# Kernel tuning notes

Hardware: AMD Instinct MI355X
Metric: run time of the kernel (lower is better)

Reference implementation:

```python
import jax, jax.numpy as jnp
import numpy as np

D_MODEL, NUM_HEADS, ROPE_DIM = 256, 8, 16
B_GRAPHS, N_MAX = 16, 512


def _make_batch():
    # ragged graph sizes between 256 and 512 atoms; contiguous, sorted ids
    sizes = np.array([256 + (i * 256) // 15 for i in range(B_GRAPHS)], dtype=np.int64)
    return np.repeat(np.arange(B_GRAPHS), sizes)  # total N = 6137


def setup_inputs() -> dict:
    key = jax.random.key(0)
    ks = jax.random.split(key, 6)
    batch_np = _make_batch()
    N = int(batch_np.shape[0])
    x = jax.random.normal(ks[0], (N, D_MODEL), jnp.float32)
    pos = jax.random.normal(ks[1], (N, 3), jnp.float32) * 3.0
    W_qkv = jax.random.normal(ks[2], (D_MODEL, 3 * D_MODEL), jnp.float32) / np.sqrt(D_MODEL).astype(np.float32)
    W_out = jax.random.normal(ks[3], (D_MODEL, D_MODEL), jnp.float32) / np.sqrt(D_MODEL).astype(np.float32)
    rope_freqs = jax.random.normal(ks[4], (ROPE_DIM,), jnp.float32) * 0.1
    W_rope = jax.random.normal(ks[5], (ROPE_DIM, NUM_HEADS), jnp.float32) / np.sqrt(ROPE_DIM).astype(np.float32)
    gamma = jnp.ones((D_MODEL,), jnp.float32)
    beta = jnp.zeros((D_MODEL,), jnp.float32)
    return {"x": x, "pos": pos, "batch": jnp.asarray(batch_np, jnp.int32),
            "W_qkv": W_qkv, "W_out": W_out, "rope_freqs": rope_freqs,
            "W_rope": W_rope, "gamma": gamma, "beta": beta,
            "B": B_GRAPHS, "n_max": N_MAX}


def _forward(x, pos, W_qkv, W_out, rope_freqs, W_rope, gamma, beta, batch, B, n_max):
    N, d = x.shape
    H = W_rope.shape[1]
    hd = d // H
    scale = hd ** -0.5
    # pad ragged graphs to [B, n_max] via vectorized scatter (batch is sorted)
    sizes = jax.ops.segment_sum(jnp.ones((N,), jnp.int32), batch, num_segments=B)
    offsets = jnp.concatenate([jnp.zeros((1,), jnp.int32), jnp.cumsum(sizes)[:-1].astype(jnp.int32)])
    pidx = jnp.arange(N, dtype=jnp.int32) - offsets[batch]  # position within graph
    x_pad = jnp.zeros((B, n_max, d), x.dtype).at[batch, pidx].set(x)
    pos_pad = jnp.zeros((B, n_max, 3), pos.dtype).at[batch, pidx].set(pos)
    pad = jnp.ones((B, n_max), bool).at[batch, pidx].set(False)  # True = padding
    # multi-head self-attention on scalar channel
    qkv = x_pad @ W_qkv  # [B, n, 3d]
    q, k, v = jnp.split(qkv, 3, axis=-1)
    heads = lambda t: t.reshape(B, n_max, H, hd).transpose(0, 2, 1, 3)  # [B,H,n,hd]
    q, k, v = heads(q), heads(k), heads(v)
    logits = jnp.einsum('bhid,bhjd->bhij', q, k) * scale
    # Euclidean RoPE distance bias: rope_proj(cos(|omega| * ||r_i - r_j||))
    diff = pos_pad[:, :, None, :] - pos_pad[:, None, :, :]  # [B,n,n,3]
    sq = jnp.sum(diff * diff, axis=-1)
    dist = jnp.where(sq > 0, jnp.sqrt(jnp.where(sq > 0, sq, 1.0)), 0.0)  # safe norm
    fourier = jnp.cos(dist[..., None] * jnp.abs(rope_freqs))  # [B,n,n,r]
    bias = jnp.einsum('bijr,rh->bhij', fourier, W_rope)
    pair_pad = (pad[:, :, None] | pad[:, None, :])[:, None]  # [B,1,n,n]
    bias = jnp.where(pair_pad, 0.0, bias)
    logits = jnp.where(pad[:, None, None, :], -1e9, logits + bias)
    attn = jax.nn.softmax(logits, axis=-1)
    out = jnp.einsum('bhij,bhjd->bhid', attn, v)
    out = out.transpose(0, 2, 1, 3).reshape(B, n_max, d) @ W_out
    out_flat = out[batch, pidx]  # gather back to flat node list
    # residual + LayerNorm (eps = 1e-5)
    y = x + out_flat
    mu = jnp.mean(y, axis=-1, keepdims=True)
    var = jnp.mean((y - mu) ** 2, axis=-1, keepdims=True)
    return gamma * (y - mu) * jax.lax.rsqrt(var + 1e-5) + beta


def reference(x, pos, batch, W_qkv, W_out, rope_freqs, W_rope, gamma, beta, B, n_max):
    return _forward(x, pos, W_qkv, W_out, rope_freqs, W_rope, gamma, beta, batch, B, n_max)
```

## Files before the change

### kernel.cpp

```cpp
#include <hip/hip_runtime.h>
#include <hip/hip_bf16.h>

typedef __hip_bfloat16 bf16;
typedef short bf16x8 __attribute__((ext_vector_type(8)));
typedef float f32x4 __attribute__((ext_vector_type(4)));

#define NGRAPH 16
#define QSCALE 0.17677669529663687f
#define VT_LD 8192

__device__ __forceinline__ bf16x8 ldcvt8(const float* p) {
  float4 u = *(const float4*)p, v = *(const float4*)(p + 4);
  __align__(16) bf16 tmp[8];
  tmp[0] = __float2bfloat16(u.x); tmp[1] = __float2bfloat16(u.y);
  tmp[2] = __float2bfloat16(u.z); tmp[3] = __float2bfloat16(u.w);
  tmp[4] = __float2bfloat16(v.x); tmp[5] = __float2bfloat16(v.y);
  tmp[6] = __float2bfloat16(v.z); tmp[7] = __float2bfloat16(v.w);
  return *(const bf16x8*)tmp;
}

__global__ __launch_bounds__(256) void k_pre(const float* __restrict__ Wqkv,
                                             const float* __restrict__ Wout,
                                             const int* __restrict__ batch,
                                             bf16* __restrict__ Wqkv_t,
                                             bf16* __restrict__ Wout_t,
                                             int* __restrict__ offs, int N) {
  __shared__ float ld[64][65];
  int bid = blockIdx.x, t = threadIdx.x;
  int c = t & 63, r0 = t >> 6;
  if (bid < 48) {
    int k0 = (bid & 3) * 64, n0 = (bid >> 2) * 64;
    #pragma unroll
    for (int r = r0; r < 64; r += 4) ld[r][c] = Wqkv[(size_t)(k0 + r) * 768 + n0 + c];
    __syncthreads();
    #pragma unroll
    for (int r = r0; r < 64; r += 4)
      Wqkv_t[(size_t)(n0 + r) * 256 + k0 + c] = __float2bfloat16(ld[c][r]);
  } else if (bid < 64) {
    int b2 = bid - 48;
    int k0 = (b2 & 3) * 64, n0 = (b2 >> 2) * 64;
    #pragma unroll
    for (int r = r0; r < 64; r += 4) ld[r][c] = Wout[(size_t)(k0 + r) * 256 + n0 + c];
    __syncthreads();
    #pragma unroll
    for (int r = r0; r < 64; r += 4)
      Wout_t[(size_t)(n0 + r) * 256 + k0 + c] = __float2bfloat16(ld[c][r]);
  } else {
    for (int i = t; i < N; i += 256) {
      if (i == 0) { offs[0] = 0; offs[NGRAPH] = N; }
      else if (batch[i] != batch[i - 1]) offs[batch[i]] = i;
    }
  }
}

__global__ __launch_bounds__(256) void k_gemm(const float* __restrict__ x,
                                              const bf16* __restrict__ Wqkv_t,
                                              const int* __restrict__ batch,
                                              const int* __restrict__ offs,
                                              bf16* __restrict__ QKVb,
                                              bf16* __restrict__ VT,
                                              int N, int MBm) {
  __shared__ float tr[64][65];
  __shared__ int rowcol[64];
  int t = threadIdx.x, bid = blockIdx.x;
  int w = t >> 6, l = t & 63, fr = l & 15, fq = l >> 4;
  int m0 = (bid % MBm) * 64, n0 = (bid / MBm) * 64;
  bool isV = (n0 >= 512);
  if (isV && t < 64) {
    int m = m0 + t; if (m > N - 1) m = N - 1;
    int b = batch[m];
    rowcol[t] = b * 512 + (m - offs[b]);
  }
  int arow = m0 + w * 16 + fr; if (arow > N - 1) arow = N - 1;
  bf16x8 af[8];
  #pragma unroll
  for (int kt = 0; kt < 8; ++kt)
    af[kt] = ldcvt8(x + (size_t)arow * 256 + kt * 32 + fq * 8);
  f32x4 acc[4];
  #pragma unroll
  for (int nt = 0; nt < 4; ++nt) acc[nt] = (f32x4){0.f, 0.f, 0.f, 0.f};
  #pragma unroll
  for (int nt = 0; nt < 4; ++nt) {
    int brow = n0 + nt * 16 + fr;
    #pragma unroll
    for (int kt = 0; kt < 8; ++kt) {
      bf16x8 bf_ = *(const bf16x8*)(Wqkv_t + (size_t)brow * 256 + kt * 32 + fq * 8);
      acc[nt] = __builtin_amdgcn_mfma_f32_16x16x32_bf16(af[kt], bf_, acc[nt], 0, 0, 0);
    }
  }
  #pragma unroll
  for (int nt = 0; nt < 4; ++nt) {
    int col = n0 + nt * 16 + fr;
    float sc = (col < 256) ? QSCALE : 1.f;
    #pragma unroll
    for (int rr = 0; rr < 4; ++rr) {
      int m = m0 + w * 16 + fq * 4 + rr;
      if (m < N) QKVb[(size_t)m * 768 + col] = __float2bfloat16(acc[nt][rr] * sc);
    }
  }
  if (isV) {
    #pragma unroll
    for (int nt = 0; nt < 4; ++nt)
      #pragma unroll
      for (int rr = 0; rr < 4; ++rr)
        tr[nt * 16 + fr][w * 16 + fq * 4 + rr] = acc[nt][rr];
    __syncthreads();
    int c = t >> 2, r0 = (t & 3) * 16;
    int dg = (n0 - 512) + c;
    #pragma unroll
    for (int i = 0; i < 16; ++i) {
      int r = r0 + i;
      VT[(size_t)dg * VT_LD + rowcol[r]] = __float2bfloat16(tr[c][r]);
    }
  }
}

__global__ __launch_bounds__(256) void k_attn(const float* __restrict__ pos,
                                              const float* __restrict__ freqs,
                                              const float* __restrict__ Wrope,
                                              const bf16* __restrict__ QKVb,
                                              const bf16* __restrict__ VT,
                                              const int* __restrict__ offs,
                                              bf16* __restrict__ Ob) {
  __shared__ float Sb[2][4][16][36];
  __shared__ __align__(16) bf16 Pt[4][16][40];
  int b = blockIdx.y, hbase = blockIdx.z * 4;
  int off = offs[b], n = offs[b + 1] - off;
  int q0 = blockIdx.x * 16;
  if (q0 >= n) return;
  int t = threadIdx.x, w = t >> 6, l = t & 63, fr = l & 15, fq = l >> 4;
  int h = hbase + w;
  const bf16* Kb = QKVb + (size_t)off * 768 + 256 + h * 32 + fq * 8;
  const bf16* Vb = VT + (size_t)(h * 32 + fr) * VT_LD + b * 512 + fq * 8;
  int qrow = q0 + fr; bool qv = qrow < n;
  bf16x8 aq = *(const bf16x8*)(QKVb + (size_t)(qv ? off + qrow : off) * 768 + h * 32 + fq * 8);
  if (!qv) aq = (bf16x8){0, 0, 0, 0, 0, 0, 0, 0};

  int bq = t >> 5, bj = t & 31;
  float qpx[2], qpy[2], qpz[2]; bool bqv[2];
  #pragma unroll
  for (int e = 0; e < 2; ++e) {
    int qq = q0 + bq + 8 * e; bqv[e] = qq < n;
    int a = (bqv[e] ? off + qq : off) * 3;
    qpx[e] = pos[a]; qpy[e] = pos[a + 1]; qpz[e] = pos[a + 2];
  }

  f32x4 Oa[2];
  Oa[0] = (f32x4){0.f, 0.f, 0.f, 0.f}; Oa[1] = (f32x4){0.f, 0.f, 0.f, 0.f};
  float lacc[4] = {0.f, 0.f, 0.f, 0.f};
  int jtiles = (n + 31) >> 5;

#define PRODUCE(JT, BUF) do {                                                     \
    int _jg = (JT) * 32 + bj; bool _vj = _jg < n;                                 \
    int _a = (_vj ? off + _jg : off) * 3;                                         \
    float _jx = pos[_a], _jy = pos[_a + 1], _jz = pos[_a + 2];                    \
    _Pragma("unroll")                                                             \
    for (int _e = 0; _e < 2; ++_e) {                                              \
      float _b0 = 0.f, _b1 = 0.f, _b2 = 0.f, _b3 = 0.f;                           \
      if (_vj && bqv[_e]) {                                                       \
        float _dx = qpx[_e] - _jx, _dy = qpy[_e] - _jy, _dz = qpz[_e] - _jz;      \
        float _d = sqrtf(_dx * _dx + _dy * _dy + _dz * _dz);                      \
        _Pragma("unroll")                                                         \
        for (int _r = 0; _r < 16; ++_r) {                                         \
          float _cv = __cosf(_d * fabsf(freqs[_r]));                              \
          _b0 += _cv * Wrope[_r * 8 + hbase + 0];                                 \
          _b1 += _cv * Wrope[_r * 8 + hbase + 1];                                 \
          _b2 += _cv * Wrope[_r * 8 + hbase + 2];                                 \
          _b3 += _cv * Wrope[_r * 8 + hbase + 3];                                 \
        }                                                                         \
      }                                                                           \
      int _qi = bq + 8 * _e;                                                      \
      Sb[BUF][0][_qi][bj] = _vj ? _b0 : -1e30f;                                   \
      Sb[BUF][1][_qi][bj] = _vj ? _b1 : -1e30f;                                   \
      Sb[BUF][2][_qi][bj] = _vj ? _b2 : -1e30f;                                   \
      Sb[BUF][3][_qi][bj] = _vj ? _b3 : -1e30f;                                   \
    }                                                                             \
  } while (0)

#define LOADT(JT, K0_, K1_, V0_, V1_) do {                                        \
    int _jt = (JT); int _k0 = _jt * 32 + fr, _k1 = _k0 + 16;                      \
    K0_ = *(const bf16x8*)(Kb + (size_t)((_k0 < n) ? _k0 : 0) * 768);             \
    K1_ = *(const bf16x8*)(Kb + (size_t)((_k1 < n) ? _k1 : 0) * 768);             \
    V0_ = *(const bf16x8*)(Vb + _jt * 32);                                        \
    V1_ = *(const bf16x8*)(Vb + (size_t)16 * VT_LD + _jt * 32);                   \
  } while (0)

  bf16x8 ck0, ck1, cv0, cv1;
  LOADT(0, ck0, ck1, cv0, cv1);
  PRODUCE(0, 0);
  __syncthreads();
  for (int jt = 0; jt < jtiles; ++jt) {
    int par = jt & 1;
    bf16x8 nk0, nk1, nv0, nv1;
    if (jt + 1 < jtiles) {
      LOADT(jt + 1, nk0, nk1, nv0, nv1);
      PRODUCE(jt + 1, par ^ 1);
    }
    f32x4 z = {0.f, 0.f, 0.f, 0.f};
    f32x4 S0 = __builtin_amdgcn_mfma_f32_16x16x32_bf16(aq, ck0, z, 0, 0, 0);
    f32x4 S1 = __builtin_amdgcn_mfma_f32_16x16x32_bf16(aq, ck1, z, 0, 0, 0);
    #pragma unroll
    for (int k = 0; k < 8; ++k) {
      int jti = k >> 2, rr = k & 3;
      float s = (jti ? S1[rr] : S0[rr]) + Sb[par][w][fq * 4 + rr][jti * 16 + fr];
      float p = __expf(s);
      lacc[rr] += p;
      Pt[w][fq * 4 + rr][jti * 16 + fr] = __float2bfloat16(p);
    }
    bf16x8 ap = *(const bf16x8*)&Pt[w][fr][fq * 8];
    Oa[0] = __builtin_amdgcn_mfma_f32_16x16x32_bf16(ap, cv0, Oa[0], 0, 0, 0);
    Oa[1] = __builtin_amdgcn_mfma_f32_16x16x32_bf16(ap, cv1, Oa[1], 0, 0, 0);
    ck0 = nk0; ck1 = nk1; cv0 = nv0; cv1 = nv1;
    __syncthreads();
  }
#undef LOADT
#undef PRODUCE
  #pragma unroll
  for (int rr = 0; rr < 4; ++rr) {
    #pragma unroll
    for (int m2 = 1; m2 <= 8; m2 <<= 1) lacc[rr] += __shfl_xor(lacc[rr], m2);
  }
  #pragma unroll
  for (int dh = 0; dh < 2; ++dh)
    #pragma unroll
    for (int rr = 0; rr < 4; ++rr) {
      int row = q0 + fq * 4 + rr;
      if (row < n)
        Ob[(size_t)(off + row) * 256 + h * 32 + dh * 16 + fr] =
            __float2bfloat16(Oa[dh][rr] / lacc[rr]);
    }
}

__global__ __launch_bounds__(256) void k_out_ln(const bf16* __restrict__ A,
                                                const bf16* __restrict__ Bt,
                                                const float* __restrict__ x,
                                                const float* __restrict__ gamma,
                                                const float* __restrict__ beta,
                                                float* __restrict__ out, int M) {
  __shared__ float ps[4][16], pss[4][16];
  int t = threadIdx.x, w = t >> 6, l = t & 63, fr = l & 15, fq = l >> 4;
  int m0 = blockIdx.x * 16;
  int arow = m0 + fr; if (arow > M - 1) arow = M - 1;
  bf16x8 af[8];
  #pragma unroll
  for (int kt = 0; kt < 8; ++kt)
    af[kt] = *(const bf16x8*)(A + (size_t)arow * 256 + kt * 32 + fq * 8);
  f32x4 acc[4];
  #pragma unroll
  for (int nt = 0; nt < 4; ++nt) {
    acc[nt] = (f32x4){0.f, 0.f, 0.f, 0.f};
    int brow = w * 64 + nt * 16 + fr;
    #pragma unroll
    for (int kt = 0; kt < 8; ++kt) {
      bf16x8 bf_ = *(const bf16x8*)(Bt + (size_t)brow * 256 + kt * 32 + fq * 8);
      acc[nt] = __builtin_amdgcn_mfma_f32_16x16x32_bf16(af[kt], bf_, acc[nt], 0, 0, 0);
    }
  }
  float y[4][4];
  #pragma unroll
  for (int rr = 0; rr < 4; ++rr) {
    int row = m0 + fq * 4 + rr;
    int rc = (row < M) ? row : (M - 1);
    float s = 0.f, ss = 0.f;
    #pragma unroll
    for (int nt = 0; nt < 4; ++nt) {
      float v = acc[nt][rr] + x[(size_t)rc * 256 + w * 64 + nt * 16 + fr];
      y[rr][nt] = v; s += v; ss += v * v;
    }
    #pragma unroll
    for (int m2 = 1; m2 <= 8; m2 <<= 1) { s += __shfl_xor(s, m2); ss += __shfl_xor(ss, m2); }
    if (fr == 0) { ps[w][fq * 4 + rr] = s; pss[w][fq * 4 + rr] = ss; }
  }
  __syncthreads();
  #pragma unroll
  for (int rr = 0; rr < 4; ++rr) {
    int row = m0 + fq * 4 + rr;
    int ri = fq * 4 + rr;
    float s = ps[0][ri] + ps[1][ri] + ps[2][ri] + ps[3][ri];
    float ss = pss[0][ri] + pss[1][ri] + pss[2][ri] + pss[3][ri];
    float mean = s * (1.f / 256.f);
    float var = ss * (1.f / 256.f) - mean * mean;
    float rstd = rsqrtf(var + 1e-5f);
    if (row < M) {
      #pragma unroll
      for (int nt = 0; nt < 4; ++nt) {
        int col = w * 64 + nt * 16 + fr;
        out[(size_t)row * 256 + col] = gamma[col] * (y[rr][nt] - mean) * rstd + beta[col];
      }
    }
  }
}

extern "C" void kernel_launch(void* const* d_in, const int* in_sizes, int n_in,
                              void* d_out, int out_size, void* d_ws, size_t ws_size,
                              hipStream_t stream) {
  (void)n_in; (void)out_size; (void)ws_size;
  const float* x     = (const float*)d_in[0];
  const float* pos   = (const float*)d_in[1];
  const int*   batch = (const int*)d_in[2];
  const float* Wqkv  = (const float*)d_in[3];
  const float* Wout  = (const float*)d_in[4];
  const float* freqs = (const float*)d_in[5];
  const float* Wrope = (const float*)d_in[6];
  const float* gamma = (const float*)d_in[7];
  const float* beta  = (const float*)d_in[8];
  float* out = (float*)d_out;

  int N = in_sizes[0] / 256;

  char* base = (char*)d_ws;
  int*   offs   = (int*)base;
  bf16*  QKVb   = (bf16*)(base + 1024);
  bf16*  VT     = (bf16*)(base + 9427456);
  bf16*  Wqkv_t = (bf16*)(base + 13621760);
  bf16*  Wout_t = (bf16*)(base + 14014976);
  bf16*  Ob     = (bf16*)(base + 14146048);

  int MBm = (N + 63) / 64;
  k_pre<<<65, 256, 0, stream>>>(Wqkv, Wout, batch, Wqkv_t, Wout_t, offs, N);
  k_gemm<<<MBm * 12, 256, 0, stream>>>(x, Wqkv_t, batch, offs, QKVb, VT, N, MBm);
  k_attn<<<dim3(32, NGRAPH, 2), 256, 0, stream>>>(pos, freqs, Wrope, QKVb, VT, offs, Ob);
  k_out_ln<<<(N + 15) / 16, 256, 0, stream>>>(Ob, Wout_t, x, gamma, beta, out, N);
}
```

Before: 181.4 us.

## Split attention key range across two blocks and merge partials in output GEMM

Splits each attention block's key-tile loop into two halves handled by separate blocks (split-K / flash-decoding style), doubling grid parallelism. Unnormalized fp32 partial outputs and row sums are written to workspace, and the output-projection kernel sums the two halves and normalizes before converting to bf16. This relies on there being no max subtraction in the softmax, so partials combine by plain addition. It adds fp32 partial traffic and a larger workspace in exchange for better occupancy on the attention kernel.

```diff
diff --git a/kernel.cpp b/kernel.cpp
--- a/kernel.cpp
+++ b/kernel.cpp
@@ -121,10 +121,14 @@
                                               const bf16* __restrict__ QKVb,
                                               const bf16* __restrict__ VT,
                                               const int* __restrict__ offs,
-                                              bf16* __restrict__ Ob) {
+                                              float* __restrict__ Op,
+                                              float* __restrict__ lp, int N) {
   __shared__ float Sb[2][4][16][36];
   __shared__ __align__(16) bf16 Pt[4][16][40];
-  int b = blockIdx.y, hbase = blockIdx.z * 4;
+  int b = blockIdx.y;
+  int zc = blockIdx.z;
+  int hbase = (zc & 1) * 4;
+  int jc = zc >> 1;
   int off = offs[b], n = offs[b + 1] - off;
   int q0 = blockIdx.x * 16;
   if (q0 >= n) return;
@@ -149,6 +153,7 @@
   Oa[0] = (f32x4){0.f, 0.f, 0.f, 0.f}; Oa[1] = (f32x4){0.f, 0.f, 0.f, 0.f};
   float lacc[4] = {0.f, 0.f, 0.f, 0.f};
   int jtiles = (n + 31) >> 5;
+  int jt0 = (jtiles * jc) >> 1, jt1 = (jtiles * (jc + 1)) >> 1;
 
 #define PRODUCE(JT, BUF) do {                                                     \
     int _jg = (JT) * 32 + bj; bool _vj = _jg < n;                                 \
@@ -186,13 +191,13 @@
   } while (0)
 
   bf16x8 ck0, ck1, cv0, cv1;
-  LOADT(0, ck0, ck1, cv0, cv1);
-  PRODUCE(0, 0);
+  LOADT(jt0, ck0, ck1, cv0, cv1);
+  PRODUCE(jt0, 0);
   __syncthreads();
-  for (int jt = 0; jt < jtiles; ++jt) {
-    int par = jt & 1;
+  for (int jt = jt0; jt < jt1; ++jt) {
+    int par = (jt - jt0) & 1;
     bf16x8 nk0, nk1, nv0, nv1;
-    if (jt + 1 < jtiles) {
+    if (jt + 1 < jt1) {
       LOADT(jt + 1, nk0, nk1, nv0, nv1);
       PRODUCE(jt + 1, par ^ 1);
     }
@@ -220,18 +225,22 @@
     #pragma unroll
     for (int m2 = 1; m2 <= 8; m2 <<= 1) lacc[rr] += __shfl_xor(lacc[rr], m2);
   }
-  #pragma unroll
-  for (int dh = 0; dh < 2; ++dh)
-    #pragma unroll
-    for (int rr = 0; rr < 4; ++rr) {
-      int row = q0 + fq * 4 + rr;
-      if (row < n)
-        Ob[(size_t)(off + row) * 256 + h * 32 + dh * 16 + fr] =
-            __float2bfloat16(Oa[dh][rr] / lacc[rr]);
-    }
-}
-
-__global__ __launch_bounds__(256) void k_out_ln(const bf16* __restrict__ A,
+  float* Opc = Op + (size_t)jc * N * 256;
+  float* lpc = lp + (size_t)jc * N * 8;
+  #pragma unroll
+  for (int rr = 0; rr < 4; ++rr) {
+    int row = q0 + fq * 4 + rr;
+    if (row < n) {
+      #pragma unroll
+      for (int dh = 0; dh < 2; ++dh)
+        Opc[(size_t)(off + row) * 256 + h * 32 + dh * 16 + fr] = Oa[dh][rr];
+      if (fr == 0) lpc[(size_t)(off + row) * 8 + h] = lacc[rr];
+    }
+  }
+}
+
+__global__ __launch_bounds__(256) void k_out_ln(const float* __restrict__ Op,
+                                                const float* __restrict__ lp,
                                                 const bf16* __restrict__ Bt,
                                                 const float* __restrict__ x,
                                                 const float* __restrict__ gamma,
@@ -241,10 +250,37 @@
   int t = threadIdx.x, w = t >> 6, l = t & 63, fr = l & 15, fq = l >> 4;
   int m0 = blockIdx.x * 16;
   int arow = m0 + fr; if (arow > M - 1) arow = M - 1;
+  const float* Op0 = Op;
+  const float* Op1 = Op + (size_t)M * 256;
+  float linv[8];
+  {
+    float4 a0 = *(const float4*)(lp + (size_t)arow * 8);
+    float4 a1 = *(const float4*)(lp + (size_t)arow * 8 + 4);
+    float4 b0 = *(const float4*)(lp + (size_t)(M + arow) * 8);
+    float4 b1 = *(const float4*)(lp + (size_t)(M + arow) * 8 + 4);
+    linv[0] = 1.f / (a0.x + b0.x); linv[1] = 1.f / (a0.y + b0.y);
+    linv[2] = 1.f / (a0.z + b0.z); linv[3] = 1.f / (a0.w + b0.w);
+    linv[4] = 1.f / (a1.x + b1.x); linv[5] = 1.f / (a1.y + b1.y);
+    linv[6] = 1.f / (a1.z + b1.z); linv[7] = 1.f / (a1.w + b1.w);
+  }
   bf16x8 af[8];
   #pragma unroll
-  for (int kt = 0; kt < 8; ++kt)
-    af[kt] = *(const bf16x8*)(A + (size_t)arow * 256 + kt * 32 + fq * 8);
+  for (int kt = 0; kt < 8; ++kt) {
+    size_t o = (size_t)arow * 256 + kt * 32 + fq * 8;
+    float4 u0 = *(const float4*)(Op0 + o),     v0 = *(const float4*)(Op0 + o + 4);
+    float4 u1 = *(const float4*)(Op1 + o),     v1 = *(const float4*)(Op1 + o + 4);
+    float li = linv[kt];
+    __align__(16) bf16 tmp[8];
+    tmp[0] = __float2bfloat16((u0.x + u1.x) * li);
+    tmp[1] = __float2bfloat16((u0.y + u1.y) * li);
+    tmp[2] = __float2bfloat16((u0.z + u1.z) * li);
+    tmp[3] = __float2bfloat16((u0.w + u1.w) * li);
+    tmp[4] = __float2bfloat16((v0.x + v1.x) * li);
+    tmp[5] = __float2bfloat16((v0.y + v1.y) * li);
+    tmp[6] = __float2bfloat16((v0.z + v1.z) * li);
+    tmp[7] = __float2bfloat16((v0.w + v1.w) * li);
+    af[kt] = *(const bf16x8*)tmp;
+  }
   f32x4 acc[4];
   #pragma unroll
   for (int nt = 0; nt < 4; ++nt) {
@@ -314,11 +350,12 @@
   bf16*  VT     = (bf16*)(base + 9427456);
   bf16*  Wqkv_t = (bf16*)(base + 13621760);
   bf16*  Wout_t = (bf16*)(base + 14014976);
-  bf16*  Ob     = (bf16*)(base + 14146048);
+  float* Op     = (float*)(base + 14146048);
+  float* lp     = (float*)(base + 26714624);
 
   int MBm = (N + 63) / 64;
   k_pre<<<65, 256, 0, stream>>>(Wqkv, Wout, batch, Wqkv_t, Wout_t, offs, N);
   k_gemm<<<MBm * 12, 256, 0, stream>>>(x, Wqkv_t, batch, offs, QKVb, VT, N, MBm);
-  k_attn<<<dim3(32, NGRAPH, 2), 256, 0, stream>>>(pos, freqs, Wrope, QKVb, VT, offs, Ob);
-  k_out_ln<<<(N + 15) / 16, 256, 0, stream>>>(Ob, Wout_t, x, gamma, beta, out, N);
-}
+  k_attn<<<dim3(32, NGRAPH, 4), 256, 0, stream>>>(pos, freqs, Wrope, QKVb, VT, offs, Op, lp, N);
+  k_out_ln<<<(N + 15) / 16, 256, 0, stream>>>(Op, lp, Wout_t, x, gamma, beta, out, N);
+}
```

Result: no change. 184.4 us (+1.7%).
